# Kernel optimization log

Measured on AMD Instinct MI355X. Metric: run time of the kernel, lower is better.

Reference implementation:

```python
import jax, jax.numpy as jnp
import numpy as np

N_NODES = 50000


def _gcn_conv(x, W, b, src, dst, n_nodes):
    """PyG GCNConv: add self-loops, symmetric deg^-1/2 norm, linear, aggregate, bias."""
    # add self-loops
    loop = jnp.arange(n_nodes, dtype=src.dtype)
    s = jnp.concatenate([src, loop])  # [E+N]
    d = jnp.concatenate([dst, loop])  # [E+N]
    # degree of A + I computed over targets
    deg = jax.ops.segment_sum(jnp.ones_like(d, dtype=x.dtype), d, num_segments=n_nodes)
    dinv = jnp.where(deg > 0, jax.lax.rsqrt(deg), 0.0)
    norm = dinv[s] * dinv[d]  # [E+N]
    h = x @ W  # [N, out] transform-first (in_dim >= out_dim friendly)
    msg = h[s] * norm[:, None]  # [E+N, out]
    out = jax.ops.segment_sum(msg, d, num_segments=n_nodes)
    return out + b


def setup_inputs() -> dict:
    key = jax.random.key(0)
    k1, k2, k3, k4 = jax.random.split(key, 4)
    in_dim, hidden, out_dim = 256, 128, 64
    E = 800000
    x = jax.random.normal(k1, (N_NODES, in_dim), dtype=jnp.float32)
    edge_index = jax.random.randint(k2, (2, E), 0, N_NODES, dtype=jnp.int64)
    W1 = jax.random.normal(k3, (in_dim, hidden), dtype=jnp.float32) / np.sqrt(in_dim)
    b1 = jnp.zeros((hidden,), dtype=jnp.float32)
    W2 = jax.random.normal(k4, (hidden, out_dim), dtype=jnp.float32) / np.sqrt(hidden)
    b2 = jnp.zeros((out_dim,), dtype=jnp.float32)
    return {"x": x, "edge_index": edge_index, "W1": W1, "b1": b1, "W2": W2, "b2": b2}


def reference(x, edge_index, W1, b1, W2, b2):
    src, dst = edge_index[0], edge_index[1]
    h = _gcn_conv(x, W1, b1, src, dst, N_NODES)
    h = jax.nn.relu(h)
    out = _gcn_conv(h, W2, b2, src, dst, N_NODES)
    return out
```

## Files before the change

kernel.cpp:

```cpp
#include <hip/hip_runtime.h>

#define N_NODES 50000
#define NCH 256
#define NBKT 256

typedef short bf16x8 __attribute__((ext_vector_type(8)));
typedef float f32x4 __attribute__((ext_vector_type(4)));

__device__ inline unsigned short f2bf(float f) {
    union { float f; unsigned u; } v; v.f = f;
    unsigned u = v.u;
    unsigned lsb = (u >> 16) & 1u;
    u += 0x7fffu + lsb;
    return (unsigned short)(u >> 16);
}

__device__ inline float bf2f(unsigned short h) {
    union { unsigned u; float f; } v; v.u = ((unsigned)h) << 16;
    return v.f;
}

__global__ __launch_bounds__(256) void prep(const int* __restrict__ dst,
                                            int* __restrict__ cnt, int E, int epc,
                                            const float* __restrict__ W1,
                                            const float* __restrict__ W2,
                                            unsigned short* __restrict__ B1h,
                                            unsigned short* __restrict__ B1l,
                                            unsigned short* __restrict__ B2h,
                                            unsigned short* __restrict__ B2l) {
    const int c = blockIdx.x;
    if (c < NCH) {
        __shared__ int h[NBKT];
        h[threadIdx.x] = 0;
        __syncthreads();
        const int e0 = c * epc;
        const int e1 = min(E, e0 + epc);
        for (int e = e0 + threadIdx.x; e < e1; e += 256)
            atomicAdd(&h[dst[e] >> 8], 1);
        __syncthreads();
        cnt[c * NBKT + threadIdx.x] = h[threadIdx.x];
        return;
    }
    int i = (c - NCH) * 256 + threadIdx.x;
    const float* W;
    unsigned short *Th, *Tl;
    int K, logM, idx;
    if (i < 32768) { W = W1; Th = B1h; Tl = B1l; K = 256; logM = 7; idx = i; }
    else if (i < 32768 + 8192) { W = W2; Th = B2h; Tl = B2l; K = 128; logM = 6; idx = i - 32768; }
    else return;
    const int M = 1 << logM;
    const int KS = K / 32;
    int k = idx >> logM;
    int n = idx & (M - 1);
    float v = W[idx];
    unsigned short h = f2bf(v);
    unsigned short l = f2bf(v - bf2f(h));
    int g = n >> 4, n16 = n & 15, ks = k >> 5, quad = (k >> 3) & 3, j = k & 7;
    size_t o = ((size_t)((g * KS + ks) * 64 + quad * 16 + n16)) * 8 + j;
    Th[o] = h;
    Tl[o] = l;
}

__global__ __launch_bounds__(256) void bkt_scan_chunks(const int* __restrict__ cnt,
                                                       int* __restrict__ off,
                                                       int* __restrict__ total) {
    __shared__ int sh[256];
    const int b = blockIdx.x;
    const int t = threadIdx.x;
    int v = cnt[t * NBKT + b];
    sh[t] = v;
    __syncthreads();
    for (int o = 1; o < 256; o <<= 1) {
        int u = (t >= o) ? sh[t - o] : 0;
        __syncthreads();
        sh[t] += u;
        __syncthreads();
    }
    off[t * NBKT + b] = sh[t] - v;
    if (t == 255) total[b] = sh[255];
}

__global__ __launch_bounds__(256) void bkt_scatter(const int* __restrict__ src,
                                                   const int* __restrict__ dst,
                                                   const int* __restrict__ off,
                                                   const int* __restrict__ total,
                                                   unsigned* __restrict__ pairs,
                                                   int E, int epc) {
    __shared__ int sh[256];
    __shared__ int cur[NBKT];
    const int c = blockIdx.x;
    const int t = threadIdx.x;
    int v = total[t];
    sh[t] = v;
    __syncthreads();
    for (int o = 1; o < 256; o <<= 1) {
        int u = (t >= o) ? sh[t - o] : 0;
        __syncthreads();
        sh[t] += u;
        __syncthreads();
    }
    cur[t] = (sh[t] - v) + off[c * NBKT + t];
    __syncthreads();
    const int e0 = c * epc;
    const int e1 = min(E, e0 + epc);
    for (int e = e0 + t; e < e1; e += 256) {
        int s = src[e];
        int d = dst[e];
        int pos = atomicAdd(&cur[d >> 8], 1);
        pairs[pos] = ((unsigned)s << 8) | (unsigned)(d & 255);
    }
}

__global__ __launch_bounds__(256) void bkt_csr(const unsigned* __restrict__ pairs,
                                               const int* __restrict__ total,
                                               int* __restrict__ rowptr,
                                               int* __restrict__ csr_src,
                                               float* __restrict__ dinv, int N) {
    __shared__ int lh[256];
    __shared__ int sc[256];
    __shared__ int lcur[256];
    const int b = blockIdx.x;
    const int t = threadIdx.x;

    sc[t] = total[t];
    __syncthreads();
    for (int o = 1; o < 256; o <<= 1) {
        int u = (t >= o) ? sc[t - o] : 0;
        __syncthreads();
        sc[t] += u;
        __syncthreads();
    }
    const int eend = sc[b];
    const int ebase = eend - total[b];
    const int node0 = b << 8;

    lh[t] = 0;
    __syncthreads();
    for (int e = ebase + t; e < eend; e += 256)
        atomicAdd(&lh[pairs[e] & 255u], 1);
    __syncthreads();
    int v = lh[t];
    sc[t] = v;
    __syncthreads();
    for (int o = 1; o < 256; o <<= 1) {
        int u = (t >= o) ? sc[t - o] : 0;
        __syncthreads();
        sc[t] += u;
        __syncthreads();
    }
    const int excl = sc[t] - v;
    lcur[t] = ebase + excl;
    const int node = node0 + t;
    if (node <= N) {
        rowptr[node] = ebase + excl;
        if (node < N) dinv[node] = rsqrtf((float)(v + 1));
    }
    __syncthreads();
    for (int e = ebase + t; e < eend; e += 256) {
        unsigned p = pairs[e];
        int pos = atomicAdd(&lcur[p & 255u], 1);
        csr_src[pos] = (int)(p >> 8);
    }
}

template <int K, int M>
__global__ __launch_bounds__(M * 4) void gemm_mfma_v4(const float* __restrict__ A,
                                                      const unsigned short* __restrict__ Bfh,
                                                      const unsigned short* __restrict__ Bfl,
                                                      const float* __restrict__ dinv,
                                                      unsigned short* __restrict__ Cb, int N) {
    const int KS = K / 32;
    const int THREADS = M * 4;
    const int CPT = 512 / THREADS;
    const int PL = 64 * 40;
    const int CPAIRS = M / 32;

    __shared__ __align__(16) unsigned short Ah[2 * PL];
    __shared__ __align__(16) unsigned short Al[2 * PL];

    const int tid = threadIdx.x;
    const int wave = tid >> 6;
    const int lane = tid & 63;
    const int n16 = lane & 15;
    const int quad = lane >> 4;
    const int cpair = wave & (CPAIRS - 1);
    const int rpair = wave / CPAIRS;
    const int row0 = blockIdx.x * 64;

    bf16x8 bh[2][2], bl[2][2];
    auto loadB = [&](int ks, int par) {
#pragma unroll
        for (int ct = 0; ct < 2; ct++) {
            const int g = cpair * 2 + ct;
            const size_t o = ((size_t)(g * KS + ks) * 64 + lane) * 8;
            bh[par][ct] = *(const bf16x8*)(Bfh + o);
            bl[par][ct] = *(const bf16x8*)(Bfl + o);
        }
    };
    loadB(0, 0);

    int srow[CPT], sc4[CPT];
    const float* aptr[CPT];
#pragma unroll
    for (int p = 0; p < CPT; p++) {
        int q = p * THREADS + tid;
        srow[p] = q >> 3;
        sc4[p] = q & 7;
        int grow = row0 + srow[p];
        if (grow >= N) grow = N - 1;
        aptr[p] = A + (size_t)grow * K + sc4[p] * 4;
    }

    float4 pre[CPT];
#pragma unroll
    for (int p = 0; p < CPT; p++) pre[p] = *(const float4*)(aptr[p]);

#pragma unroll
    for (int p = 0; p < CPT; p++) {
        ushort4 h4, l4;
        unsigned short* hp = (unsigned short*)&h4;
        unsigned short* lp = (unsigned short*)&l4;
        float av[4] = {pre[p].x, pre[p].y, pre[p].z, pre[p].w};
#pragma unroll
        for (int j = 0; j < 4; j++) {
            unsigned short h = f2bf(av[j]);
            hp[j] = h;
            lp[j] = f2bf(av[j] - bf2f(h));
        }
        *(ushort4*)(Ah + srow[p] * 40 + sc4[p] * 4) = h4;
        *(ushort4*)(Al + srow[p] * 40 + sc4[p] * 4) = l4;
    }
    if (KS > 1) {
#pragma unroll
        for (int p = 0; p < CPT; p++) pre[p] = *(const float4*)(aptr[p] + 32);
    }
    __syncthreads();

    f32x4 acc[2][2] = {};

#pragma unroll
    for (int ks = 0; ks < KS; ks++) {
        const int cur = ks & 1;
        if (ks + 1 < KS) loadB(ks + 1, cur ^ 1);
#pragma unroll
        for (int rt = 0; rt < 2; rt++) {
            const int ro = cur * PL + (rpair * 32 + rt * 16 + n16) * 40 + quad * 8;
            bf16x8 ah = *(const bf16x8*)(Ah + ro);
            bf16x8 al = *(const bf16x8*)(Al + ro);
#pragma unroll
            for (int ct = 0; ct < 2; ct++) {
                acc[rt][ct] = __builtin_amdgcn_mfma_f32_16x16x32_bf16(ah, bh[cur][ct], acc[rt][ct], 0, 0, 0);
                acc[rt][ct] = __builtin_amdgcn_mfma_f32_16x16x32_bf16(ah, bl[cur][ct], acc[rt][ct], 0, 0, 0);
                acc[rt][ct] = __builtin_amdgcn_mfma_f32_16x16x32_bf16(al, bh[cur][ct], acc[rt][ct], 0, 0, 0);
            }
        }
        if (ks + 1 < KS) {
            const int nxt = (cur ^ 1) * PL;
#pragma unroll
            for (int p = 0; p < CPT; p++) {
                ushort4 h4, l4;
                unsigned short* hp = (unsigned short*)&h4;
                unsigned short* lp = (unsigned short*)&l4;
                float av[4] = {pre[p].x, pre[p].y, pre[p].z, pre[p].w};
#pragma unroll
                for (int j = 0; j < 4; j++) {
                    unsigned short h = f2bf(av[j]);
                    hp[j] = h;
                    lp[j] = f2bf(av[j] - bf2f(h));
                }
                *(ushort4*)(Ah + nxt + srow[p] * 40 + sc4[p] * 4) = h4;
                *(ushort4*)(Al + nxt + srow[p] * 40 + sc4[p] * 4) = l4;
            }
            if (ks + 2 < KS) {
#pragma unroll
                for (int p = 0; p < CPT; p++)
                    pre[p] = *(const float4*)(aptr[p] + (ks + 2) * 32);
            }
        }
        __syncthreads();
    }

#pragma unroll
    for (int rt = 0; rt < 2; rt++) {
#pragma unroll
        for (int ct = 0; ct < 2; ct++) {
            const int col = cpair * 32 + ct * 16 + n16;
            const int rbase = row0 + rpair * 32 + rt * 16 + quad * 4;
#pragma unroll
            for (int r = 0; r < 4; r++) {
                int orow = rbase + r;
                if (orow < N) {
                    Cb[(size_t)orow * M + col] = f2bf(dinv[orow] * acc[rt][ct][r]);
                }
            }
        }
    }
}

template <int K, int M>
__global__ __launch_bounds__(1024) void gather_gemm2(const unsigned short* __restrict__ hnb,
                                                     const int* __restrict__ rowptr,
                                                     const int* __restrict__ csr_src,
                                                     const float* __restrict__ dinv,
                                                     const float* __restrict__ bias,
                                                     const unsigned short* __restrict__ Bfh,
                                                     const unsigned short* __restrict__ Bfl,
                                                     unsigned short* __restrict__ Cb, int N) {
    const int KS = K / 32;
    const int CPAIRS = M / 32;
    const int PLP = 64 * 40;

    __shared__ __align__(16) unsigned short Ah[KS * PLP];

    const int tid = threadIdx.x;
    const int wave = tid >> 6;
    const int lane = tid & 63;
    const int n16 = lane & 15;
    const int quad = lane >> 4;
    const int cpair = wave & (CPAIRS - 1);
    const int rpair = (wave / CPAIRS) & 1;
    const int row0 = blockIdx.x * 64;

    bf16x8 bh[2][2], bl[2][2];
    auto loadB = [&](int ks, int par) {
#pragma unroll
        for (int ct = 0; ct < 2; ct++) {
            const int g = cpair * 2 + ct;
            const size_t o = ((size_t)(g * KS + ks) * 64 + lane) * 8;
            bh[par][ct] = *(const bf16x8*)(Bfh + o);
            bl[par][ct] = *(const bf16x8*)(Bfl + o);
        }
    };
    if (wave < 4) loadB(0, 0);

    {
        const int j = tid & 15;
        const int r = tid >> 4;
        const int panel = j >> 2;
        const int coff = (j & 3) * 8;
        const int g = row0 + r;
        unsigned short* ldst = Ah + panel * PLP + r * 40 + coff;
        if (g < N) {
            float acc[8];
            {
                bf16x8 v = *(const bf16x8*)(hnb + (size_t)g * K + j * 8);
#pragma unroll
                for (int i = 0; i < 8; i++) acc[i] = bf2f((unsigned short)v[i]);
            }
            int e = rowptr[g];
            const int end = rowptr[g + 1];
            for (; e + 3 < end; e += 4) {
                int s0 = csr_src[e];
                int s1 = csr_src[e + 1];
                int s2 = csr_src[e + 2];
                int s3 = csr_src[e + 3];
                bf16x8 v0 = *(const bf16x8*)(hnb + (size_t)s0 * K + j * 8);
                bf16x8 v1 = *(const bf16x8*)(hnb + (size_t)s1 * K + j * 8);
                bf16x8 v2 = *(const bf16x8*)(hnb + (size_t)s2 * K + j * 8);
                bf16x8 v3 = *(const bf16x8*)(hnb + (size_t)s3 * K + j * 8);
#pragma unroll
                for (int i = 0; i < 8; i++) {
                    acc[i] += (bf2f((unsigned short)v0[i]) + bf2f((unsigned short)v1[i])) +
                              (bf2f((unsigned short)v2[i]) + bf2f((unsigned short)v3[i]));
                }
            }
            for (; e < end; e++) {
                int s0 = csr_src[e];
                bf16x8 v0 = *(const bf16x8*)(hnb + (size_t)s0 * K + j * 8);
#pragma unroll
                for (int i = 0; i < 8; i++) acc[i] += bf2f((unsigned short)v0[i]);
            }
            const float s = dinv[g];
            bf16x8 rr;
#pragma unroll
            for (int i = 0; i < 8; i++)
                rr[i] = (short)f2bf(fmaxf(s * acc[i] + bias[j * 8 + i], 0.0f));
            *(bf16x8*)ldst = rr;
        } else {
            bf16x8 z = {};
            *(bf16x8*)ldst = z;
        }
    }
    __syncthreads();
    if (wave >= 4) return;

    f32x4 acc[2][2] = {};
#pragma unroll
    for (int ks = 0; ks < KS; ks++) {
        const int cur = ks & 1;
        if (ks + 1 < KS) loadB(ks + 1, cur ^ 1);
#pragma unroll
        for (int rt = 0; rt < 2; rt++) {
            const int ro = ks * PLP + (rpair * 32 + rt * 16 + n16) * 40 + quad * 8;
            bf16x8 ah = *(const bf16x8*)(Ah + ro);
#pragma unroll
            for (int ct = 0; ct < 2; ct++) {
                acc[rt][ct] = __builtin_amdgcn_mfma_f32_16x16x32_bf16(ah, bh[cur][ct], acc[rt][ct], 0, 0, 0);
                acc[rt][ct] = __builtin_amdgcn_mfma_f32_16x16x32_bf16(ah, bl[cur][ct], acc[rt][ct], 0, 0, 0);
            }
        }
    }

#pragma unroll
    for (int rt = 0; rt < 2; rt++) {
#pragma unroll
        for (int ct = 0; ct < 2; ct++) {
            const int col = cpair * 32 + ct * 16 + n16;
            const int rbase = row0 + rpair * 32 + rt * 16 + quad * 4;
#pragma unroll
            for (int r = 0; r < 4; r++) {
                int orow = rbase + r;
                if (orow < N) {
                    Cb[(size_t)orow * M + col] = f2bf(dinv[orow] * acc[rt][ct][r]);
                }
            }
        }
    }
}

template <int M>
__global__ __launch_bounds__(256) void gather_to_f32(const unsigned short* __restrict__ hnb,
                                                     const int* __restrict__ rowptr,
                                                     const int* __restrict__ csr_src,
                                                     const float* __restrict__ dinv,
                                                     const float* __restrict__ bias,
                                                     float* __restrict__ outp, int n) {
    const int MQ = M / 8;
    const int GPB = 256 / MQ;
    int g = blockIdx.x * GPB + threadIdx.x / MQ;
    int j = threadIdx.x % MQ;
    if (g >= n) return;

    float acc[8];
    {
        bf16x8 v = *(const bf16x8*)(hnb + (size_t)g * M + j * 8);
#pragma unroll
        for (int i = 0; i < 8; i++) acc[i] = bf2f((unsigned short)v[i]);
    }

    int e = rowptr[g];
    const int end = rowptr[g + 1];
    for (; e + 3 < end; e += 4) {
        int s0 = csr_src[e];
        int s1 = csr_src[e + 1];
        int s2 = csr_src[e + 2];
        int s3 = csr_src[e + 3];
        bf16x8 v0 = *(const bf16x8*)(hnb + (size_t)s0 * M + j * 8);
        bf16x8 v1 = *(const bf16x8*)(hnb + (size_t)s1 * M + j * 8);
        bf16x8 v2 = *(const bf16x8*)(hnb + (size_t)s2 * M + j * 8);
        bf16x8 v3 = *(const bf16x8*)(hnb + (size_t)s3 * M + j * 8);
#pragma unroll
        for (int i = 0; i < 8; i++) {
            acc[i] += (bf2f((unsigned short)v0[i]) + bf2f((unsigned short)v1[i])) +
                      (bf2f((unsigned short)v2[i]) + bf2f((unsigned short)v3[i]));
        }
    }
    for (; e < end; e++) {
        int s0 = csr_src[e];
        bf16x8 v0 = *(const bf16x8*)(hnb + (size_t)s0 * M + j * 8);
#pragma unroll
        for (int i = 0; i < 8; i++) acc[i] += bf2f((unsigned short)v0[i]);
    }

    const float s = dinv[g];
    float r[8];
#pragma unroll
    for (int i = 0; i < 8; i++) r[i] = s * acc[i] + bias[j * 8 + i];
    float* op = outp + (size_t)g * M + j * 8;
    *(float4*)(op) = make_float4(r[0], r[1], r[2], r[3]);
    *(float4*)(op + 4) = make_float4(r[4], r[5], r[6], r[7]);
}

extern "C" void kernel_launch(void* const* d_in, const int* in_sizes, int n_in,
                              void* d_out, int out_size, void* d_ws, size_t ws_size,
                              hipStream_t stream) {
    const float* x  = (const float*)d_in[0];
    const int*   ei = (const int*)d_in[1];
    const float* W1 = (const float*)d_in[2];
    const float* b1 = (const float*)d_in[3];
    const float* W2 = (const float*)d_in[4];
    const float* b2 = (const float*)d_in[5];

    const int N = N_NODES;
    const int E = in_sizes[1] / 2;
    const int* src = ei;
    const int* dst = ei + E;

    char* ws = (char*)d_ws;
    size_t off = 0;
    auto carve = [&](size_t bytes) {
        char* p = ws + off;
        off += (bytes + 255) & ~(size_t)255;
        return p;
    };
    int*      cnt     = (int*)     carve((size_t)NCH * NBKT * 4);
    int*      offm    = (int*)     carve((size_t)NCH * NBKT * 4);
    int*      total   = (int*)     carve((size_t)NBKT * 4);
    unsigned* pairs   = (unsigned*)carve((size_t)E * 4);
    int*      rowptr  = (int*)     carve((size_t)(N + 1) * 4);
    int*      csr_src = (int*)     carve((size_t)E * 4);
    float*    dinv    = (float*)   carve((size_t)N * 4);
    unsigned short* W1th = (unsigned short*)carve((size_t)256 * 128 * 2);
    unsigned short* W1tl = (unsigned short*)carve((size_t)256 * 128 * 2);
    unsigned short* W2th = (unsigned short*)carve((size_t)128 * 64 * 2);
    unsigned short* W2tl = (unsigned short*)carve((size_t)128 * 64 * 2);
    unsigned short* hn1b = (unsigned short*)carve((size_t)N * 128 * 2);
    unsigned short* hn2b = (unsigned short*)carve((size_t)N * 64 * 2);

    const int epc = (E + NCH - 1) / NCH;
    const int nbk = (N + 255) >> 8;

    prep<<<NCH + 160, 256, 0, stream>>>(dst, cnt, E, epc, W1, W2, W1th, W1tl, W2th, W2tl);
    bkt_scan_chunks<<<NBKT, 256, 0, stream>>>(cnt, offm, total);
    bkt_scatter<<<NCH, 256, 0, stream>>>(src, dst, offm, total, pairs, E, epc);
    bkt_csr<<<nbk, 256, 0, stream>>>(pairs, total, rowptr, csr_src, dinv, N);

    const int GB = (N + 63) / 64;

    gemm_mfma_v4<256, 128><<<GB, 512, 0, stream>>>(x, W1th, W1tl, dinv, hn1b, N);

    gather_gemm2<128, 64><<<GB, 1024, 0, stream>>>(hn1b, rowptr, csr_src, dinv, b1,
                                                   W2th, W2tl, hn2b, N);

    {
        const int GPB = 256 / (64 / 8);
        gather_to_f32<64><<<(N + GPB - 1) / GPB, 256, 0, stream>>>(
            hn2b, rowptr, csr_src, dinv, b2, (float*)d_out, N);
    }
}
```

Before: 199.4 us.

## Fuse CSR build with layer-1 GEMM and compute degree via global atomics

Per-node degrees are now counted with global atomics during the bucket scatter, so dinv no longer depends on the CSR build. The CSR build and the first GEMM are then merged into one launch, with the first nbk blocks building the CSR and the rest running the GEMM, which computes dinv from deg itself. The layer-1 output is stored as two 64-column planes. The second gather+GEMM kernel drops from 1024 to 512 threads, and each thread now gathers two 8-element chunks from those planes. This saves a launch and lets the CSR build overlap the GEMM, at the cost of 800k extra global atomics in the scatter.

```diff
diff --git a/kernel.cpp b/kernel.cpp
--- a/kernel.cpp
+++ b/kernel.cpp
@@ -63,10 +63,13 @@
 
 __global__ __launch_bounds__(256) void bkt_scan_chunks(const int* __restrict__ cnt,
                                                        int* __restrict__ off,
-                                                       int* __restrict__ total) {
+                                                       int* __restrict__ total,
+                                                       int* __restrict__ deg) {
     __shared__ int sh[256];
     const int b = blockIdx.x;
     const int t = threadIdx.x;
+    int z = b * 256 + t;
+    if (z < N_NODES) deg[z] = 0;
     int v = cnt[t * NBKT + b];
     sh[t] = v;
     __syncthreads();
@@ -85,6 +88,7 @@
                                                    const int* __restrict__ off,
                                                    const int* __restrict__ total,
                                                    unsigned* __restrict__ pairs,
+                                                   int* __restrict__ deg,
                                                    int E, int epc) {
     __shared__ int sh[256];
     __shared__ int cur[NBKT];
@@ -106,69 +110,73 @@
     for (int e = e0 + t; e < e1; e += 256) {
         int s = src[e];
         int d = dst[e];
+        atomicAdd(&deg[d], 1);
         int pos = atomicAdd(&cur[d >> 8], 1);
         pairs[pos] = ((unsigned)s << 8) | (unsigned)(d & 255);
     }
 }
 
-__global__ __launch_bounds__(256) void bkt_csr(const unsigned* __restrict__ pairs,
-                                               const int* __restrict__ total,
-                                               int* __restrict__ rowptr,
-                                               int* __restrict__ csr_src,
-                                               float* __restrict__ dinv, int N) {
-    __shared__ int lh[256];
-    __shared__ int sc[256];
-    __shared__ int lcur[256];
-    const int b = blockIdx.x;
-    const int t = threadIdx.x;
-
-    sc[t] = total[t];
-    __syncthreads();
-    for (int o = 1; o < 256; o <<= 1) {
-        int u = (t >= o) ? sc[t - o] : 0;
-        __syncthreads();
-        sc[t] += u;
-        __syncthreads();
-    }
-    const int eend = sc[b];
-    const int ebase = eend - total[b];
-    const int node0 = b << 8;
-
-    lh[t] = 0;
-    __syncthreads();
-    for (int e = ebase + t; e < eend; e += 256)
-        atomicAdd(&lh[pairs[e] & 255u], 1);
-    __syncthreads();
-    int v = lh[t];
-    sc[t] = v;
-    __syncthreads();
-    for (int o = 1; o < 256; o <<= 1) {
-        int u = (t >= o) ? sc[t - o] : 0;
-        __syncthreads();
-        sc[t] += u;
-        __syncthreads();
-    }
-    const int excl = sc[t] - v;
-    lcur[t] = ebase + excl;
-    const int node = node0 + t;
-    if (node <= N) {
-        rowptr[node] = ebase + excl;
-        if (node < N) dinv[node] = rsqrtf((float)(v + 1));
-    }
-    __syncthreads();
-    for (int e = ebase + t; e < eend; e += 256) {
-        unsigned p = pairs[e];
-        int pos = atomicAdd(&lcur[p & 255u], 1);
-        csr_src[pos] = (int)(p >> 8);
-    }
-}
-
 template <int K, int M>
-__global__ __launch_bounds__(M * 4) void gemm_mfma_v4(const float* __restrict__ A,
-                                                      const unsigned short* __restrict__ Bfh,
-                                                      const unsigned short* __restrict__ Bfl,
-                                                      const float* __restrict__ dinv,
-                                                      unsigned short* __restrict__ Cb, int N) {
+__global__ __launch_bounds__(512) void csr_gemm1(const unsigned* __restrict__ pairs,
+                                                 const int* __restrict__ total,
+                                                 int* __restrict__ rowptr,
+                                                 int* __restrict__ csr_src,
+                                                 const float* __restrict__ A,
+                                                 const unsigned short* __restrict__ Bfh,
+                                                 const unsigned short* __restrict__ Bfl,
+                                                 const int* __restrict__ deg,
+                                                 float* __restrict__ dinv,
+                                                 unsigned short* __restrict__ Cb,
+                                                 int N, int nbk) {
+    const int tid = threadIdx.x;
+    if (blockIdx.x < nbk) {
+        __shared__ int lh[256];
+        __shared__ int sc[256];
+        __shared__ int lcur[256];
+        const int b = blockIdx.x;
+        const bool a = tid < 256;
+
+        if (a) sc[tid] = total[tid];
+        __syncthreads();
+        for (int o = 1; o < 256; o <<= 1) {
+            int u = (a && tid >= o) ? sc[tid - o] : 0;
+            __syncthreads();
+            if (a) sc[tid] += u;
+            __syncthreads();
+        }
+        const int eend = sc[b];
+        const int ebase = eend - total[b];
+        const int node0 = b << 8;
+
+        if (a) lh[tid] = 0;
+        __syncthreads();
+        for (int e = ebase + tid; e < eend; e += 512)
+            atomicAdd(&lh[pairs[e] & 255u], 1);
+        __syncthreads();
+        int v = a ? lh[tid] : 0;
+        if (a) sc[tid] = v;
+        __syncthreads();
+        for (int o = 1; o < 256; o <<= 1) {
+            int u = (a && tid >= o) ? sc[tid - o] : 0;
+            __syncthreads();
+            if (a) sc[tid] += u;
+            __syncthreads();
+        }
+        if (a) {
+            const int excl = sc[tid] - v;
+            lcur[tid] = ebase + excl;
+            const int node = node0 + tid;
+            if (node <= N) rowptr[node] = ebase + excl;
+        }
+        __syncthreads();
+        for (int e = ebase + tid; e < eend; e += 512) {
+            unsigned p = pairs[e];
+            int pos = atomicAdd(&lcur[p & 255u], 1);
+            csr_src[pos] = (int)(p >> 8);
+        }
+        return;
+    }
+
     const int KS = K / 32;
     const int THREADS = M * 4;
     const int CPT = 512 / THREADS;
@@ -177,6 +185,159 @@
 
     __shared__ __align__(16) unsigned short Ah[2 * PL];
     __shared__ __align__(16) unsigned short Al[2 * PL];
+    __shared__ float sdv[64];
+
+    const int wave = tid >> 6;
+    const int lane = tid & 63;
+    const int n16 = lane & 15;
+    const int quad = lane >> 4;
+    const int cpair = wave & (CPAIRS - 1);
+    const int rpair = wave / CPAIRS;
+    const int row0 = (blockIdx.x - nbk) * 64;
+
+    if (tid < 64) {
+        int gr = row0 + tid;
+        if (gr < N) {
+            float dv = rsqrtf((float)(deg[gr] + 1));
+            sdv[tid] = dv;
+            dinv[gr] = dv;
+        } else {
+            sdv[tid] = 0.0f;
+        }
+    }
+
+    bf16x8 bh[2][2], bl[2][2];
+    auto loadB = [&](int ks, int par) {
+#pragma unroll
+        for (int ct = 0; ct < 2; ct++) {
+            const int g = cpair * 2 + ct;
+            const size_t o = ((size_t)(g * KS + ks) * 64 + lane) * 8;
+            bh[par][ct] = *(const bf16x8*)(Bfh + o);
+            bl[par][ct] = *(const bf16x8*)(Bfl + o);
+        }
+    };
+    loadB(0, 0);
+
+    int srow[CPT], sc4[CPT];
+    const float* aptr[CPT];
+#pragma unroll
+    for (int p = 0; p < CPT; p++) {
+        int q = p * THREADS + tid;
+        srow[p] = q >> 3;
+        sc4[p] = q & 7;
+        int grow = row0 + srow[p];
+        if (grow >= N) grow = N - 1;
+        aptr[p] = A + (size_t)grow * K + sc4[p] * 4;
+    }
+
+    float4 pre[CPT];
+#pragma unroll
+    for (int p = 0; p < CPT; p++) pre[p] = *(const float4*)(aptr[p]);
+
+#pragma unroll
+    for (int p = 0; p < CPT; p++) {
+        ushort4 h4, l4;
+        unsigned short* hp = (unsigned short*)&h4;
+        unsigned short* lp = (unsigned short*)&l4;
+        float av[4] = {pre[p].x, pre[p].y, pre[p].z, pre[p].w};
+#pragma unroll
+        for (int j = 0; j < 4; j++) {
+            unsigned short h = f2bf(av[j]);
+            hp[j] = h;
+            lp[j] = f2bf(av[j] - bf2f(h));
+        }
+        *(ushort4*)(Ah + srow[p] * 40 + sc4[p] * 4) = h4;
+        *(ushort4*)(Al + srow[p] * 40 + sc4[p] * 4) = l4;
+    }
+    if (KS > 1) {
+#pragma unroll
+        for (int p = 0; p < CPT; p++) pre[p] = *(const float4*)(aptr[p] + 32);
+    }
+    __syncthreads();
+
+    f32x4 acc[2][2] = {};
+
+#pragma unroll
+    for (int ks = 0; ks < KS; ks++) {
+        const int cur = ks & 1;
+        if (ks + 1 < KS) loadB(ks + 1, cur ^ 1);
+#pragma unroll
+        for (int rt = 0; rt < 2; rt++) {
+            const int ro = cur * PL + (rpair * 32 + rt * 16 + n16) * 40 + quad * 8;
+            bf16x8 ah = *(const bf16x8*)(Ah + ro);
+            bf16x8 al = *(const bf16x8*)(Al + ro);
+#pragma unroll
+            for (int ct = 0; ct < 2; ct++) {
+                acc[rt][ct] = __builtin_amdgcn_mfma_f32_16x16x32_bf16(ah, bh[cur][ct], acc[rt][ct], 0, 0, 0);
+                acc[rt][ct] = __builtin_amdgcn_mfma_f32_16x16x32_bf16(ah, bl[cur][ct], acc[rt][ct], 0, 0, 0);
+                acc[rt][ct] = __builtin_amdgcn_mfma_f32_16x16x32_bf16(al, bh[cur][ct], acc[rt][ct], 0, 0, 0);
+            }
+        }
+        if (ks + 1 < KS) {
+            const int nxt = (cur ^ 1) * PL;
+#pragma unroll
+            for (int p = 0; p < CPT; p++) {
+                ushort4 h4, l4;
+                unsigned short* hp = (unsigned short*)&h4;
+                unsigned short* lp = (unsigned short*)&l4;
+                float av[4] = {pre[p].x, pre[p].y, pre[p].z, pre[p].w};
+#pragma unroll
+                for (int j = 0; j < 4; j++) {
+                    unsigned short h = f2bf(av[j]);
+                    hp[j] = h;
+                    lp[j] = f2bf(av[j] - bf2f(h));
+                }
+                *(ushort4*)(Ah + nxt + srow[p] * 40 + sc4[p] * 4) = h4;
+                *(ushort4*)(Al + nxt + srow[p] * 40 + sc4[p] * 4) = l4;
+            }
+            if (ks + 2 < KS) {
+#pragma unroll
+                for (int p = 0; p < CPT; p++)
+                    pre[p] = *(const float4*)(aptr[p] + (ks + 2) * 32);
+            }
+        }
+        __syncthreads();
+    }
+
+#pragma unroll
+    for (int rt = 0; rt < 2; rt++) {
+#pragma unroll
+        for (int ct = 0; ct < 2; ct++) {
+            const int col = cpair * 32 + ct * 16 + n16;
+            const int rbase = row0 + rpair * 32 + rt * 16 + quad * 4;
+#pragma unroll
+            for (int r = 0; r < 4; r++) {
+                int orow = rbase + r;
+                if (orow < N) {
+                    float dv = sdv[orow - row0];
+                    unsigned short ob = f2bf(dv * acc[rt][ct][r]);
+                    if (M == 128) {
+                        size_t plane = (size_t)(col >> 6);
+                        Cb[plane * ((size_t)N_NODES * 64) + (size_t)orow * 64 + (col & 63)] = ob;
+                    } else {
+                        Cb[(size_t)orow * M + col] = ob;
+                    }
+                }
+            }
+        }
+    }
+}
+
+template <int K, int M>
+__global__ __launch_bounds__(512) void gather_gemm2(const unsigned short* __restrict__ hnb,
+                                                    const int* __restrict__ rowptr,
+                                                    const int* __restrict__ csr_src,
+                                                    const float* __restrict__ dinv,
+                                                    const float* __restrict__ bias,
+                                                    const unsigned short* __restrict__ Bfh,
+                                                    const unsigned short* __restrict__ Bfl,
+                                                    unsigned short* __restrict__ Cb, int N) {
+    const int KS = K / 32;
+    const int CPAIRS = M / 32;
+    const int PLP = 64 * 40;
+    const size_t PLANE = (size_t)N_NODES * 64;
+
+    __shared__ __align__(16) unsigned short Ah[KS * PLP];
 
     const int tid = threadIdx.x;
     const int wave = tid >> 6;
@@ -197,188 +358,55 @@
             bl[par][ct] = *(const bf16x8*)(Bfl + o);
         }
     };
-    loadB(0, 0);
-
-    int srow[CPT], sc4[CPT];
-    const float* aptr[CPT];
-#pragma unroll
-    for (int p = 0; p < CPT; p++) {
-        int q = p * THREADS + tid;
-        srow[p] = q >> 3;
-        sc4[p] = q & 7;
-        int grow = row0 + srow[p];
-        if (grow >= N) grow = N - 1;
-        aptr[p] = A + (size_t)grow * K + sc4[p] * 4;
-    }
-
-    float4 pre[CPT];
-#pragma unroll
-    for (int p = 0; p < CPT; p++) pre[p] = *(const float4*)(aptr[p]);
-
-#pragma unroll
-    for (int p = 0; p < CPT; p++) {
-        ushort4 h4, l4;
-        unsigned short* hp = (unsigned short*)&h4;
-        unsigned short* lp = (unsigned short*)&l4;
-        float av[4] = {pre[p].x, pre[p].y, pre[p].z, pre[p].w};
-#pragma unroll
-        for (int j = 0; j < 4; j++) {
-            unsigned short h = f2bf(av[j]);
-            hp[j] = h;
-            lp[j] = f2bf(av[j] - bf2f(h));
-        }
-        *(ushort4*)(Ah + srow[p] * 40 + sc4[p] * 4) = h4;
-        *(ushort4*)(Al + srow[p] * 40 + sc4[p] * 4) = l4;
-    }
-    if (KS > 1) {
-#pragma unroll
-        for (int p = 0; p < CPT; p++) pre[p] = *(const float4*)(aptr[p] + 32);
-    }
-    __syncthreads();
-
-    f32x4 acc[2][2] = {};
-
-#pragma unroll
-    for (int ks = 0; ks < KS; ks++) {
-        const int cur = ks & 1;
-        if (ks + 1 < KS) loadB(ks + 1, cur ^ 1);
-#pragma unroll
-        for (int rt = 0; rt < 2; rt++) {
-            const int ro = cur * PL + (rpair * 32 + rt * 16 + n16) * 40 + quad * 8;
-            bf16x8 ah = *(const bf16x8*)(Ah + ro);
-            bf16x8 al = *(const bf16x8*)(Al + ro);
-#pragma unroll
-            for (int ct = 0; ct < 2; ct++) {
-                acc[rt][ct] = __builtin_amdgcn_mfma_f32_16x16x32_bf16(ah, bh[cur][ct], acc[rt][ct], 0, 0, 0);
-                acc[rt][ct] = __builtin_amdgcn_mfma_f32_16x16x32_bf16(ah, bl[cur][ct], acc[rt][ct], 0, 0, 0);
-                acc[rt][ct] = __builtin_amdgcn_mfma_f32_16x16x32_bf16(al, bh[cur][ct], acc[rt][ct], 0, 0, 0);
-            }
-        }
-        if (ks + 1 < KS) {
-            const int nxt = (cur ^ 1) * PL;
-#pragma unroll
-            for (int p = 0; p < CPT; p++) {
-                ushort4 h4, l4;
-                unsigned short* hp = (unsigned short*)&h4;
-                unsigned short* lp = (unsigned short*)&l4;
-                float av[4] = {pre[p].x, pre[p].y, pre[p].z, pre[p].w};
-#pragma unroll
-                for (int j = 0; j < 4; j++) {
-                    unsigned short h = f2bf(av[j]);
-                    hp[j] = h;
-                    lp[j] = f2bf(av[j] - bf2f(h));
+    if (wave < 4) loadB(0, 0);
+
+    {
+        const int j8 = tid & 7;
+        const int r = tid >> 3;
+        const int g = row0 + r;
+        for (int p = 0; p < 2; p++) {
+            unsigned short* ldst = Ah + (2 * p + (j8 >> 2)) * PLP + r * 40 + (j8 & 3) * 8;
+            if (g < N) {
+                const unsigned short* plane = hnb + (size_t)p * PLANE + (size_t)j8 * 8;
+                float acc[8];
+                {
+                    bf16x8 v = *(const bf16x8*)(plane + (size_t)g * 64);
+#pragma unroll
+                    for (int i = 0; i < 8; i++) acc[i] = bf2f((unsigned short)v[i]);
                 }
-                *(ushort4*)(Ah + nxt + srow[p] * 40 + sc4[p] * 4) = h4;
-                *(ushort4*)(Al + nxt + srow[p] * 40 + sc4[p] * 4) = l4;
-            }
-            if (ks + 2 < KS) {
-#pragma unroll
-                for (int p = 0; p < CPT; p++)
-                    pre[p] = *(const float4*)(aptr[p] + (ks + 2) * 32);
-            }
-        }
-        __syncthreads();
-    }
-
-#pragma unroll
-    for (int rt = 0; rt < 2; rt++) {
-#pragma unroll
-        for (int ct = 0; ct < 2; ct++) {
-            const int col = cpair * 32 + ct * 16 + n16;
-            const int rbase = row0 + rpair * 32 + rt * 16 + quad * 4;
-#pragma unroll
-            for (int r = 0; r < 4; r++) {
-                int orow = rbase + r;
-                if (orow < N) {
-                    Cb[(size_t)orow * M + col] = f2bf(dinv[orow] * acc[rt][ct][r]);
+                int e = rowptr[g];
+                const int end = rowptr[g + 1];
+                for (; e + 3 < end; e += 4) {
+                    int s0 = csr_src[e];
+                    int s1 = csr_src[e + 1];
+                    int s2 = csr_src[e + 2];
+                    int s3 = csr_src[e + 3];
+                    bf16x8 v0 = *(const bf16x8*)(plane + (size_t)s0 * 64);
+                    bf16x8 v1 = *(const bf16x8*)(plane + (size_t)s1 * 64);
+                    bf16x8 v2 = *(const bf16x8*)(plane + (size_t)s2 * 64);
+                    bf16x8 v3 = *(const bf16x8*)(plane + (size_t)s3 * 64);
+#pragma unroll
+                    for (int i = 0; i < 8; i++) {
+                        acc[i] += (bf2f((unsigned short)v0[i]) + bf2f((unsigned short)v1[i])) +
+                                  (bf2f((unsigned short)v2[i]) + bf2f((unsigned short)v3[i]));
+                    }
                 }
-            }
-        }
-    }
-}
-
-template <int K, int M>
-__global__ __launch_bounds__(1024) void gather_gemm2(const unsigned short* __restrict__ hnb,
-                                                     const int* __restrict__ rowptr,
-                                                     const int* __restrict__ csr_src,
-                                                     const float* __restrict__ dinv,
-                                                     const float* __restrict__ bias,
-                                                     const unsigned short* __restrict__ Bfh,
-                                                     const unsigned short* __restrict__ Bfl,
-                                                     unsigned short* __restrict__ Cb, int N) {
-    const int KS = K / 32;
-    const int CPAIRS = M / 32;
-    const int PLP = 64 * 40;
-
-    __shared__ __align__(16) unsigned short Ah[KS * PLP];
-
-    const int tid = threadIdx.x;
-    const int wave = tid >> 6;
-    const int lane = tid & 63;
-    const int n16 = lane & 15;
-    const int quad = lane >> 4;
-    const int cpair = wave & (CPAIRS - 1);
-    const int rpair = (wave / CPAIRS) & 1;
-    const int row0 = blockIdx.x * 64;
-
-    bf16x8 bh[2][2], bl[2][2];
-    auto loadB = [&](int ks, int par) {
-#pragma unroll
-        for (int ct = 0; ct < 2; ct++) {
-            const int g = cpair * 2 + ct;
-            const size_t o = ((size_t)(g * KS + ks) * 64 + lane) * 8;
-            bh[par][ct] = *(const bf16x8*)(Bfh + o);
-            bl[par][ct] = *(const bf16x8*)(Bfl + o);
-        }
-    };
-    if (wave < 4) loadB(0, 0);
-
-    {
-        const int j = tid & 15;
-        const int r = tid >> 4;
-        const int panel = j >> 2;
-        const int coff = (j & 3) * 8;
-        const int g = row0 + r;
-        unsigned short* ldst = Ah + panel * PLP + r * 40 + coff;
-        if (g < N) {
-            float acc[8];
-            {
-                bf16x8 v = *(const bf16x8*)(hnb + (size_t)g * K + j * 8);
-#pragma unroll
-                for (int i = 0; i < 8; i++) acc[i] = bf2f((unsigned short)v[i]);
-            }
-            int e = rowptr[g];
-            const int end = rowptr[g + 1];
-            for (; e + 3 < end; e += 4) {
-                int s0 = csr_src[e];
-                int s1 = csr_src[e + 1];
-                int s2 = csr_src[e + 2];
-                int s3 = csr_src[e + 3];
-                bf16x8 v0 = *(const bf16x8*)(hnb + (size_t)s0 * K + j * 8);
-                bf16x8 v1 = *(const bf16x8*)(hnb + (size_t)s1 * K + j * 8);
-                bf16x8 v2 = *(const bf16x8*)(hnb + (size_t)s2 * K + j * 8);
-                bf16x8 v3 = *(const bf16x8*)(hnb + (size_t)s3 * K + j * 8);
-#pragma unroll
-                for (int i = 0; i < 8; i++) {
-                    acc[i] += (bf2f((unsigned short)v0[i]) + bf2f((unsigned short)v1[i])) +
-                              (bf2f((unsigned short)v2[i]) + bf2f((unsigned short)v3[i]));
+                for (; e < end; e++) {
+                    int s0 = csr_src[e];
+                    bf16x8 v0 = *(const bf16x8*)(plane + (size_t)s0 * 64);
+#pragma unroll
+                    for (int i = 0; i < 8; i++) acc[i] += bf2f((unsigned short)v0[i]);
                 }
-            }
-            for (; e < end; e++) {
-                int s0 = csr_src[e];
-                bf16x8 v0 = *(const bf16x8*)(hnb + (size_t)s0 * K + j * 8);
-#pragma unroll
-                for (int i = 0; i < 8; i++) acc[i] += bf2f((unsigned short)v0[i]);
-            }
-            const float s = dinv[g];
-            bf16x8 rr;
-#pragma unroll
-            for (int i = 0; i < 8; i++)
-                rr[i] = (short)f2bf(fmaxf(s * acc[i] + bias[j * 8 + i], 0.0f));
-            *(bf16x8*)ldst = rr;
-        } else {
-            bf16x8 z = {};
-            *(bf16x8*)ldst = z;
+                const float s = dinv[g];
+                bf16x8 rr;
+#pragma unroll
+                for (int i = 0; i < 8; i++)
+                    rr[i] = (short)f2bf(fmaxf(s * acc[i] + bias[p * 64 + j8 * 8 + i], 0.0f));
+                *(bf16x8*)ldst = rr;
+            } else {
+                bf16x8 z = {};
+                *(bf16x8*)ldst = z;
+            }
         }
     }
     __syncthreads();
@@ -500,6 +528,7 @@
     int*      rowptr  = (int*)     carve((size_t)(N + 1) * 4);
     int*      csr_src = (int*)     carve((size_t)E * 4);
     float*    dinv    = (float*)   carve((size_t)N * 4);
+    int*      deg     = (int*)     carve((size_t)N * 4);
     unsigned short* W1th = (unsigned short*)carve((size_t)256 * 128 * 2);
     unsigned short* W1tl = (unsigned short*)carve((size_t)256 * 128 * 2);
     unsigned short* W2th = (unsigned short*)carve((size_t)128 * 64 * 2);
@@ -509,19 +538,15 @@
 
     const int epc = (E + NCH - 1) / NCH;
     const int nbk = (N + 255) >> 8;
+    const int GB = (N + 63) / 64;
 
     prep<<<NCH + 160, 256, 0, stream>>>(dst, cnt, E, epc, W1, W2, W1th, W1tl, W2th, W2tl);
-    bkt_scan_chunks<<<NBKT, 256, 0, stream>>>(cnt, offm, total);
-    bkt_scatter<<<NCH, 256, 0, stream>>>(src, dst, offm, total, pairs, E, epc);
-    bkt_csr<<<nbk, 256, 0, stream>>>(pairs, total, rowptr, csr_src, dinv, N);
-
-    const int GB = (N + 63) / 64;
-
-    gemm_mfma_v4<256, 128><<<GB, 512, 0, stream>>>(x, W1th, W1tl, dinv, hn1b, N);
-
-    gather_gemm2<128, 64><<<GB, 1024, 0, stream>>>(hn1b, rowptr, csr_src, dinv, b1,
-                                                   W2th, W2tl, hn2b, N);
-
+    bkt_scan_chunks<<<NBKT, 256, 0, stream>>>(cnt, offm, total, deg);
+    bkt_scatter<<<NCH, 256, 0, stream>>>(src, dst, offm, total, pairs, deg, E, epc);
+    csr_gemm1<256, 128><<<nbk + GB, 512, 0, stream>>>(pairs, total, rowptr, csr_src,
+                                                      x, W1th, W1tl, deg, dinv, hn1b, N, nbk);
+    gather_gemm2<128, 64><<<GB, 512, 0, stream>>>(hn1b, rowptr, csr_src, dinv, b1,
+                                                  W2th, W2tl, hn2b, N);
     {
         const int GPB = 256 / (64 / 8);
         gather_to_f32<64><<<(N + GPB - 1) / GPB, 256, 0, stream>>>(
```

Result: slower. 219.4 us (+10.0%).

## Store hidden features in 32-column planes and gather plane by plane

Applied to the files above, without the earlier changes.

The intermediate bf16 feature matrices are now written as column planes of 32 features (64 bytes per row per plane) instead of row-major, so each sparse gather pass only touches a narrower working set that fits better in cache. The fused gather+GEMM kernel drops to 512 threads, splits each row's edge list between two threads and combines partial sums through shared memory, looping over planes with barriers. The final gather kernel also iterates over planes. The cost is re-reading csr_src once per plane and extra synchronisation.

```diff
diff --git a/kernel.cpp b/kernel.cpp
--- a/kernel.cpp
+++ b/kernel.cpp
@@ -290,7 +290,9 @@
             for (int r = 0; r < 4; r++) {
                 int orow = rbase + r;
                 if (orow < N) {
-                    Cb[(size_t)orow * M + col] = f2bf(dinv[orow] * acc[rt][ct][r]);
+                    unsigned short ob = f2bf(dinv[orow] * acc[rt][ct][r]);
+                    Cb[(size_t)(col >> 5) * ((size_t)N_NODES * 32) +
+                       (size_t)orow * 32 + (col & 31)] = ob;
                 }
             }
         }
@@ -298,19 +300,22 @@
 }
 
 template <int K, int M>
-__global__ __launch_bounds__(1024) void gather_gemm2(const unsigned short* __restrict__ hnb,
-                                                     const int* __restrict__ rowptr,
-                                                     const int* __restrict__ csr_src,
-                                                     const float* __restrict__ dinv,
-                                                     const float* __restrict__ bias,
-                                                     const unsigned short* __restrict__ Bfh,
-                                                     const unsigned short* __restrict__ Bfl,
-                                                     unsigned short* __restrict__ Cb, int N) {
+__global__ __launch_bounds__(512) void gather_gemm2(const unsigned short* __restrict__ hnb,
+                                                    const int* __restrict__ rowptr,
+                                                    const int* __restrict__ csr_src,
+                                                    const float* __restrict__ dinv,
+                                                    const float* __restrict__ bias,
+                                                    const unsigned short* __restrict__ Bfh,
+                                                    const unsigned short* __restrict__ Bfl,
+                                                    unsigned short* __restrict__ Cb, int N) {
     const int KS = K / 32;
     const int CPAIRS = M / 32;
     const int PLP = 64 * 40;
+    const size_t PLANE1 = (size_t)N_NODES * 32;
+    const size_t PLANE2 = (size_t)N_NODES * 32;
 
     __shared__ __align__(16) unsigned short Ah[KS * PLP];
+    __shared__ float Psum[64 * 4 * 8];
 
     const int tid = threadIdx.x;
     const int wave = tid >> 6;
@@ -318,7 +323,7 @@
     const int n16 = lane & 15;
     const int quad = lane >> 4;
     const int cpair = wave & (CPAIRS - 1);
-    const int rpair = (wave / CPAIRS) & 1;
+    const int rpair = wave / CPAIRS;
     const int row0 = blockIdx.x * 64;
 
     bf16x8 bh[2][2], bl[2][2];
@@ -334,54 +339,76 @@
     if (wave < 4) loadB(0, 0);
 
     {
-        const int j = tid & 15;
-        const int r = tid >> 4;
-        const int panel = j >> 2;
-        const int coff = (j & 3) * 8;
-        const int g = row0 + r;
-        unsigned short* ldst = Ah + panel * PLP + r * 40 + coff;
+        const int j4 = tid & 3;
+        const int h  = (tid >> 2) & 1;
+        const int r  = tid >> 3;
+        const int g  = row0 + r;
+        float* ps = Psum + (r * 4 + j4) * 8;
+        int e0 = 0, emid = 0, eend = 0;
+        float dv = 0.0f;
         if (g < N) {
-            float acc[8];
-            {
-                bf16x8 v = *(const bf16x8*)(hnb + (size_t)g * K + j * 8);
-#pragma unroll
-                for (int i = 0; i < 8; i++) acc[i] = bf2f((unsigned short)v[i]);
-            }
-            int e = rowptr[g];
-            const int end = rowptr[g + 1];
-            for (; e + 3 < end; e += 4) {
-                int s0 = csr_src[e];
-                int s1 = csr_src[e + 1];
-                int s2 = csr_src[e + 2];
-                int s3 = csr_src[e + 3];
-                bf16x8 v0 = *(const bf16x8*)(hnb + (size_t)s0 * K + j * 8);
-                bf16x8 v1 = *(const bf16x8*)(hnb + (size_t)s1 * K + j * 8);
-                bf16x8 v2 = *(const bf16x8*)(hnb + (size_t)s2 * K + j * 8);
-                bf16x8 v3 = *(const bf16x8*)(hnb + (size_t)s3 * K + j * 8);
-#pragma unroll
-                for (int i = 0; i < 8; i++) {
-                    acc[i] += (bf2f((unsigned short)v0[i]) + bf2f((unsigned short)v1[i])) +
-                              (bf2f((unsigned short)v2[i]) + bf2f((unsigned short)v3[i]));
-                }
-            }
-            for (; e < end; e++) {
-                int s0 = csr_src[e];
-                bf16x8 v0 = *(const bf16x8*)(hnb + (size_t)s0 * K + j * 8);
-#pragma unroll
-                for (int i = 0; i < 8; i++) acc[i] += bf2f((unsigned short)v0[i]);
-            }
-            const float s = dinv[g];
-            bf16x8 rr;
-#pragma unroll
-            for (int i = 0; i < 8; i++)
-                rr[i] = (short)f2bf(fmaxf(s * acc[i] + bias[j * 8 + i], 0.0f));
-            *(bf16x8*)ldst = rr;
-        } else {
-            bf16x8 z = {};
-            *(bf16x8*)ldst = z;
-        }
-    }
-    __syncthreads();
+            e0 = rowptr[g];
+            eend = rowptr[g + 1];
+            emid = e0 + ((eend - e0) >> 1);
+            dv = dinv[g];
+        }
+        for (int p = 0; p < KS; p++) {
+            float acc[8] = {0.f, 0.f, 0.f, 0.f, 0.f, 0.f, 0.f, 0.f};
+            if (g < N) {
+                const unsigned short* plane = hnb + (size_t)p * PLANE1 + j4 * 8;
+                int e, ee;
+                if (h == 0) {
+                    bf16x8 v = *(const bf16x8*)(plane + (size_t)g * 32);
+#pragma unroll
+                    for (int i = 0; i < 8; i++) acc[i] = bf2f((unsigned short)v[i]);
+                    e = e0; ee = emid;
+                } else {
+                    e = emid; ee = eend;
+                }
+                for (; e + 3 < ee; e += 4) {
+                    int s0 = csr_src[e];
+                    int s1 = csr_src[e + 1];
+                    int s2 = csr_src[e + 2];
+                    int s3 = csr_src[e + 3];
+                    bf16x8 v0 = *(const bf16x8*)(plane + (size_t)s0 * 32);
+                    bf16x8 v1 = *(const bf16x8*)(plane + (size_t)s1 * 32);
+                    bf16x8 v2 = *(const bf16x8*)(plane + (size_t)s2 * 32);
+                    bf16x8 v3 = *(const bf16x8*)(plane + (size_t)s3 * 32);
+#pragma unroll
+                    for (int i = 0; i < 8; i++) {
+                        acc[i] += (bf2f((unsigned short)v0[i]) + bf2f((unsigned short)v1[i])) +
+                                  (bf2f((unsigned short)v2[i]) + bf2f((unsigned short)v3[i]));
+                    }
+                }
+                for (; e < ee; e++) {
+                    int s0 = csr_src[e];
+                    bf16x8 v0 = *(const bf16x8*)(plane + (size_t)s0 * 32);
+#pragma unroll
+                    for (int i = 0; i < 8; i++) acc[i] += bf2f((unsigned short)v0[i]);
+                }
+            }
+            if (h == 1) {
+#pragma unroll
+                for (int i = 0; i < 8; i++) ps[i] = acc[i];
+            }
+            __syncthreads();
+            if (h == 0) {
+                unsigned short* ldst = Ah + p * PLP + r * 40 + j4 * 8;
+                bf16x8 rr;
+                if (g < N) {
+#pragma unroll
+                    for (int i = 0; i < 8; i++) {
+                        float t = dv * (acc[i] + ps[i]) + bias[p * 32 + j4 * 8 + i];
+                        rr[i] = (short)f2bf(fmaxf(t, 0.0f));
+                    }
+                } else {
+                    rr = bf16x8{};
+                }
+                *(bf16x8*)ldst = rr;
+            }
+            __syncthreads();
+        }
+    }
     if (wave >= 4) return;
 
     f32x4 acc[2][2] = {};
@@ -411,7 +438,8 @@
             for (int r = 0; r < 4; r++) {
                 int orow = rbase + r;
                 if (orow < N) {
-                    Cb[(size_t)orow * M + col] = f2bf(dinv[orow] * acc[rt][ct][r]);
+                    unsigned short ob = f2bf(dinv[orow] * acc[rt][ct][r]);
+                    Cb[(size_t)(col >> 5) * PLANE2 + (size_t)orow * 32 + (col & 31)] = ob;
                 }
             }
         }
@@ -425,50 +453,56 @@
                                                      const float* __restrict__ dinv,
                                                      const float* __restrict__ bias,
                                                      float* __restrict__ outp, int n) {
-    const int MQ = M / 8;
+    const int NP = M / 32;
+    const int MQ = 4;
     const int GPB = 256 / MQ;
+    const size_t PLANE = (size_t)N_NODES * 32;
     int g = blockIdx.x * GPB + threadIdx.x / MQ;
     int j = threadIdx.x % MQ;
     if (g >= n) return;
 
-    float acc[8];
-    {
-        bf16x8 v = *(const bf16x8*)(hnb + (size_t)g * M + j * 8);
-#pragma unroll
-        for (int i = 0; i < 8; i++) acc[i] = bf2f((unsigned short)v[i]);
-    }
-
-    int e = rowptr[g];
-    const int end = rowptr[g + 1];
-    for (; e + 3 < end; e += 4) {
-        int s0 = csr_src[e];
-        int s1 = csr_src[e + 1];
-        int s2 = csr_src[e + 2];
-        int s3 = csr_src[e + 3];
-        bf16x8 v0 = *(const bf16x8*)(hnb + (size_t)s0 * M + j * 8);
-        bf16x8 v1 = *(const bf16x8*)(hnb + (size_t)s1 * M + j * 8);
-        bf16x8 v2 = *(const bf16x8*)(hnb + (size_t)s2 * M + j * 8);
-        bf16x8 v3 = *(const bf16x8*)(hnb + (size_t)s3 * M + j * 8);
-#pragma unroll
-        for (int i = 0; i < 8; i++) {
-            acc[i] += (bf2f((unsigned short)v0[i]) + bf2f((unsigned short)v1[i])) +
-                      (bf2f((unsigned short)v2[i]) + bf2f((unsigned short)v3[i]));
-        }
-    }
-    for (; e < end; e++) {
-        int s0 = csr_src[e];
-        bf16x8 v0 = *(const bf16x8*)(hnb + (size_t)s0 * M + j * 8);
-#pragma unroll
-        for (int i = 0; i < 8; i++) acc[i] += bf2f((unsigned short)v0[i]);
-    }
-
+    const int e0 = rowptr[g];
+    const int eend = rowptr[g + 1];
     const float s = dinv[g];
-    float r[8];
-#pragma unroll
-    for (int i = 0; i < 8; i++) r[i] = s * acc[i] + bias[j * 8 + i];
-    float* op = outp + (size_t)g * M + j * 8;
-    *(float4*)(op) = make_float4(r[0], r[1], r[2], r[3]);
-    *(float4*)(op + 4) = make_float4(r[4], r[5], r[6], r[7]);
+
+    for (int p = 0; p < NP; p++) {
+        const unsigned short* plane = hnb + (size_t)p * PLANE + j * 8;
+        float acc[8];
+        {
+            bf16x8 v = *(const bf16x8*)(plane + (size_t)g * 32);
+#pragma unroll
+            for (int i = 0; i < 8; i++) acc[i] = bf2f((unsigned short)v[i]);
+        }
+        int e = e0;
+        for (; e + 3 < eend; e += 4) {
+            int s0 = csr_src[e];
+            int s1 = csr_src[e + 1];
+            int s2 = csr_src[e + 2];
+            int s3 = csr_src[e + 3];
+            bf16x8 v0 = *(const bf16x8*)(plane + (size_t)s0 * 32);
+            bf16x8 v1 = *(const bf16x8*)(plane + (size_t)s1 * 32);
+            bf16x8 v2 = *(const bf16x8*)(plane + (size_t)s2 * 32);
+            bf16x8 v3 = *(const bf16x8*)(plane + (size_t)s3 * 32);
+#pragma unroll
+            for (int i = 0; i < 8; i++) {
+                acc[i] += (bf2f((unsigned short)v0[i]) + bf2f((unsigned short)v1[i])) +
+                          (bf2f((unsigned short)v2[i]) + bf2f((unsigned short)v3[i]));
+            }
+        }
+        for (; e < eend; e++) {
+            int s0 = csr_src[e];
+            bf16x8 v0 = *(const bf16x8*)(plane + (size_t)s0 * 32);
+#pragma unroll
+            for (int i = 0; i < 8; i++) acc[i] += bf2f((unsigned short)v0[i]);
+        }
+
+        float r[8];
+#pragma unroll
+        for (int i = 0; i < 8; i++) r[i] = s * acc[i] + bias[p * 32 + j * 8 + i];
+        float* op = outp + (size_t)g * M + p * 32 + j * 8;
+        *(float4*)(op) = make_float4(r[0], r[1], r[2], r[3]);
+        *(float4*)(op + 4) = make_float4(r[4], r[5], r[6], r[7]);
+    }
 }
 
 extern "C" void kernel_launch(void* const* d_in, const int* in_sizes, int n_in,
@@ -509,22 +543,18 @@
 
     const int epc = (E + NCH - 1) / NCH;
     const int nbk = (N + 255) >> 8;
+    const int GB = (N + 63) / 64;
 
     prep<<<NCH + 160, 256, 0, stream>>>(dst, cnt, E, epc, W1, W2, W1th, W1tl, W2th, W2tl);
     bkt_scan_chunks<<<NBKT, 256, 0, stream>>>(cnt, offm, total);
     bkt_scatter<<<NCH, 256, 0, stream>>>(src, dst, offm, total, pairs, E, epc);
     bkt_csr<<<nbk, 256, 0, stream>>>(pairs, total, rowptr, csr_src, dinv, N);
 
-    const int GB = (N + 63) / 64;
-
     gemm_mfma_v4<256, 128><<<GB, 512, 0, stream>>>(x, W1th, W1tl, dinv, hn1b, N);
 
-    gather_gemm2<128, 64><<<GB, 1024, 0, stream>>>(hn1b, rowptr, csr_src, dinv, b1,
-                                                   W2th, W2tl, hn2b, N);
-
-    {
-        const int GPB = 256 / (64 / 8);
-        gather_to_f32<64><<<(N + GPB - 1) / GPB, 256, 0, stream>>>(
-            hn2b, rowptr, csr_src, dinv, b2, (float*)d_out, N);
-    }
-}
+    gather_gemm2<128, 64><<<GB, 512, 0, stream>>>(hn1b, rowptr, csr_src, dinv, b1,
+                                                  W2th, W2tl, hn2b, N);
+
+    gather_to_f32<64><<<GB, 256, 0, stream>>>(hn2b, rowptr, csr_src, dinv, b2,
+                                              (float*)d_out, N);
+}
```

Result: slower. 221.5 us (+11.1%).
